# Performance work log

Hardware: AMD Instinct MI355X
Metric: run time of the kernel (lower is better)

## Reference

```python
import jax, jax.numpy as jnp
import numpy as np

B, S, HID, NH = 2, 2048, 1024, 16
HD = HID // NH  # head dim = 64


def setup_inputs() -> dict:
    key = jax.random.key(0)
    ks = jax.random.split(key, 8)
    sc = 0.02
    return {
        "hidden_states": jax.random.normal(ks[0], (B, S, HID), jnp.float32),
        "hidden_states2": jax.random.normal(ks[1], (B, S, HID), jnp.float32),
        "Wq": jax.random.normal(ks[2], (HID, HID), jnp.float32) * sc,
        "bq": jnp.zeros((HID,), jnp.float32),
        "Wk": jax.random.normal(ks[3], (HID, HID), jnp.float32) * sc,
        "bk": jnp.zeros((HID,), jnp.float32),
        "Wv": jax.random.normal(ks[4], (HID, HID), jnp.float32) * sc,
        "bv": jnp.zeros((HID,), jnp.float32),
    }


def _split_heads(x):
    # [B, S, HID] -> [B, NH, S, HD]
    b, s, _ = x.shape
    return x.reshape(b, s, NH, HD).transpose(0, 2, 1, 3)


def reference(hidden_states, hidden_states2, Wq, bq, Wk, bk, Wv, bv):
    # Linear layers use torch convention: y = x @ W.T + b
    q = _split_heads(hidden_states @ Wq.T + bq)    # [B,NH,Sq,HD]
    k = _split_heads(hidden_states2 @ Wk.T + bk)   # [B,NH,Sk,HD]
    v = _split_heads(hidden_states2 @ Wv.T + bv)   # [B,NH,Sk,HD]
    scores = jnp.einsum("bhqd,bhkd->bhqk", q, k) / jnp.sqrt(jnp.float32(HD))
    probs = jax.nn.softmax(scores, axis=-1)        # dropout prob = 0 (eval)
    ctx = jnp.einsum("bhqk,bhkd->bhqd", probs, v)  # [B,NH,Sq,HD]
    ctx = ctx.transpose(0, 2, 1, 3).reshape(hidden_states.shape[0], hidden_states.shape[1], HID)
    return ctx
```

## Files before the change

### kernel.cpp

```cpp
#include <hip/hip_runtime.h>
#include <hip/hip_bf16.h>
#include <stdint.h>

#define B_   2
#define S_   2048
#define HID_ 1024
#define NH_  16
#define HD_  64

typedef __attribute__((ext_vector_type(4))) float f32x4;
typedef __attribute__((ext_vector_type(8))) short bf16x8;

__device__ inline unsigned short f2bf(float x) {
    __hip_bfloat16 h = __float2bfloat16(x);
    return reinterpret_cast<unsigned short&>(h);
}

__device__ inline void gload_lds16(const void* g, void* l) {
    __builtin_amdgcn_global_load_lds(
        (const __attribute__((address_space(1))) void*)g,
        (__attribute__((address_space(3))) void*)l, 16, 0, 0);
}

__device__ inline float fast_exp2(float x) {
    float r;
    asm("v_exp_f32 %0, %1" : "=v"(r) : "v"(x));
    return r;
}

__global__ __launch_bounds__(256) void cvt_all(
    const float* __restrict__ X1, const float* __restrict__ X2,
    const float* __restrict__ Wq, const float* __restrict__ Wk, const float* __restrict__ Wv,
    unsigned short* __restrict__ X1b, unsigned short* __restrict__ X2b,
    unsigned short* __restrict__ Wqb, unsigned short* __restrict__ Wkb,
    unsigned short* __restrict__ Wvb)
{
    const int id = blockIdx.x;
    const float* src;
    unsigned short* dst;
    int base;
    if (id < 2048)      { src = X1; dst = X1b; base = id; }
    else if (id < 4096) { src = X2; dst = X2b; base = id - 2048; }
    else if (id < 4608) { src = Wq; dst = Wqb; base = id - 4096; }
    else if (id < 5120) { src = Wk; dst = Wkb; base = id - 4608; }
    else                { src = Wv; dst = Wvb; base = id - 5120; }
    const size_t off = (size_t)base * 2048 + (size_t)threadIdx.x * 8;
    float4 a = *(const float4*)&src[off];
    float4 b = *(const float4*)&src[off + 4];
    unsigned short o[8] = {f2bf(a.x), f2bf(a.y), f2bf(a.z), f2bf(a.w),
                           f2bf(b.x), f2bf(b.y), f2bf(b.z), f2bf(b.w)};
    *(uint4*)&dst[off] = *(uint4*)o;
}

__global__ __launch_bounds__(256, 3) void qkv_gemm(
    const unsigned short* __restrict__ X1b, const unsigned short* __restrict__ X2b,
    const unsigned short* __restrict__ Wqb, const unsigned short* __restrict__ Wkb,
    const unsigned short* __restrict__ Wvb,
    const float* __restrict__ bq, const float* __restrict__ bk, const float* __restrict__ bv,
    unsigned short* __restrict__ Qo, unsigned short* __restrict__ Ko, unsigned short* __restrict__ Vo)
{
    const int z = blockIdx.z;
    const unsigned short* X = (z == 0) ? X1b : X2b;
    const unsigned short* W = (z == 0) ? Wqb : (z == 1 ? Wkb : Wvb);
    const float* bias = (z == 0) ? bq : (z == 1 ? bk : bv);
    unsigned short* out = (z == 0) ? Qo : (z == 1 ? Ko : Vo);

    __shared__ __align__(16) unsigned short SM[128 * 132];
    unsigned short* As = SM;
    unsigned short* Bs = SM + 128 * 64;

    const int m0 = blockIdx.x * 128;
    const int n0 = blockIdx.y * 128;
    const int t = threadIdx.x;
    const int lane = t & 63;
    const int w = t >> 6;
    const int lo = lane & 15, hi = lane >> 4;
    const int wm = w >> 1, wn = w & 1;

    const int srow = lane >> 3;
    const int scol = ((lane & 7) ^ srow) * 8;

    f32x4 acc[4][4];
    const f32x4 fzero = {0.f, 0.f, 0.f, 0.f};
    #pragma unroll
    for (int i = 0; i < 4; ++i)
        #pragma unroll
        for (int j = 0; j < 4; ++j) acc[i][j] = fzero;

    for (int kt = 0; kt < 16; ++kt) {
        __syncthreads();
        #pragma unroll
        for (int i = 0; i < 4; ++i) {
            const int r = w * 32 + i * 8 + srow;
            gload_lds16(&X[(size_t)(m0 + r) * HID_ + kt * 64 + scol],
                        &As[w * 2048 + i * 512]);
            gload_lds16(&W[(size_t)(n0 + r) * HID_ + kt * 64 + scol],
                        &Bs[w * 2048 + i * 512]);
        }
        __syncthreads();

        #pragma unroll
        for (int s = 0; s < 2; ++s) {
            const int rcol = ((s * 4 + hi) ^ (lo & 7)) * 8;
            bf16x8 a[4], b[4];
            #pragma unroll
            for (int i = 0; i < 4; ++i) {
                a[i] = *(const bf16x8*)&As[(wm * 64 + i * 16 + lo) * 64 + rcol];
                b[i] = *(const bf16x8*)&Bs[(wn * 64 + i * 16 + lo) * 64 + rcol];
            }
            #pragma unroll
            for (int i = 0; i < 4; ++i)
                #pragma unroll
                for (int j = 0; j < 4; ++j)
                    acc[i][j] = __builtin_amdgcn_mfma_f32_16x16x32_bf16(a[i], b[j], acc[i][j], 0, 0, 0);
        }
    }

    if (z != 2) {
        const float sc = (z == 0) ? 0.18033688011112042f : 1.0f;
        #pragma unroll
        for (int i = 0; i < 4; ++i) {
            #pragma unroll
            for (int j = 0; j < 4; ++j) {
                int col = n0 + wn * 64 + j * 16 + lo;
                float bb = bias[col];
                #pragma unroll
                for (int r = 0; r < 4; ++r) {
                    int row = m0 + wm * 64 + i * 16 + hi * 4 + r;
                    out[(size_t)row * HID_ + col] = f2bf((acc[i][j][r] + bb) * sc);
                }
            }
        }
    } else {
        __syncthreads();
        unsigned short* Ts = SM;
        #pragma unroll
        for (int i = 0; i < 4; ++i) {
            #pragma unroll
            for (int j = 0; j < 4; ++j) {
                int nl = wn * 64 + j * 16 + lo;
                float bb = bias[n0 + nl];
                int ml = wm * 64 + i * 16 + hi * 4;
                ushort4 pk;
                pk.x = f2bf(acc[i][j][0] + bb);
                pk.y = f2bf(acc[i][j][1] + bb);
                pk.z = f2bf(acc[i][j][2] + bb);
                pk.w = f2bf(acc[i][j][3] + bb);
                *(ushort4*)&Ts[nl * 132 + ml] = pk;
            }
        }
        __syncthreads();
        const int nn = t >> 1;
        const int mh = (t & 1) * 64;
        const int bI = m0 >> 11;
        const int sb = (m0 & 2047) + mh;
        size_t obase = (size_t)bI * ((size_t)HID_ * S_) + (size_t)(n0 + nn) * S_ + sb;
        #pragma unroll
        for (int kk = 0; kk < 8; ++kk)
            *(uint4*)&out[obase + kk * 8] = *(const uint4*)&Ts[nn * 132 + mh + kk * 8];
    }
}

__global__ __launch_bounds__(256, 2) void attn_fwd(
    const unsigned short* __restrict__ Q, const unsigned short* __restrict__ K,
    const unsigned short* __restrict__ Vt, float* __restrict__ out)
{
    __shared__ __align__(16) unsigned short Ks[2][64 * 64];
    __shared__ __align__(16) unsigned short Vs[2][64 * 64];

    const int t = threadIdx.x;
    const int lane = t & 63;
    const int w = t >> 6;
    const int lo = lane & 15, hi = lane >> 4;

    const int id = blockIdx.x + 16 * blockIdx.y;
    const int vb = (id & 7) * 64 + (id >> 3);
    const int qt = vb & 15;
    const int bh = vb >> 4;
    const int b = bh >> 4, h = bh & 15;

    const int q0 = qt * 128;
    const size_t baseQK = (size_t)b * S_ * HID_ + (size_t)h * HD_;
    const size_t baseV  = (size_t)b * ((size_t)HID_ * S_) + (size_t)h * ((size_t)HD_ * S_);

    bf16x8 qb[2][2];
    #pragma unroll
    for (int qf = 0; qf < 2; ++qf)
        #pragma unroll
        for (int st = 0; st < 2; ++st)
            qb[qf][st] = *(const bf16x8*)&Q[baseQK + (size_t)(q0 + w * 32 + qf * 16 + lo) * HID_
                                            + st * 32 + hi * 8];

    f32x4 O[2][4];
    const f32x4 fzero = {0.f, 0.f, 0.f, 0.f};
    f32x4 lacc[2] = {fzero, fzero};
    #pragma unroll
    for (int qf = 0; qf < 2; ++qf)
        #pragma unroll
        for (int c = 0; c < 4; ++c) O[qf][c] = fzero;

    bf16x8 ones;
    #pragma unroll
    for (int j = 0; j < 4; ++j) ((unsigned*)&ones)[j] = 0x3F803F80u;

    const int srow = lane >> 3;
    const int scol = ((lane & 7) ^ srow) * 8;

    auto STAGE = [&](int buf, int kn) {
        #pragma unroll
        for (int i = 0; i < 2; ++i) {
            const int rr = w * 16 + i * 8 + srow;
            gload_lds16(&K[baseQK + (size_t)(kn + rr) * HID_ + scol],
                        &Ks[buf][w * 1024 + i * 512]);
            gload_lds16(&Vt[baseV + (size_t)rr * S_ + kn + scol],
                        &Vs[buf][w * 1024 + i * 512]);
        }
    };

    STAGE(0, 0);

    for (int tt = 0; tt < 32; ++tt) {
        const int cur = tt & 1;
        const bool pre = (tt < 31);

        __builtin_amdgcn_s_barrier();
        if (pre) STAGE(cur ^ 1, (tt + 1) * 64);

        if (pre) asm volatile("s_waitcnt vmcnt(4)" ::: "memory");
        else     asm volatile("s_waitcnt vmcnt(0)" ::: "memory");
        __builtin_amdgcn_s_barrier();
        __builtin_amdgcn_sched_barrier(0);

        const unsigned short* Kc = Ks[cur];
        const unsigned short* Vc = Vs[cur];

        f32x4 s[2][4];
        __builtin_amdgcn_s_setprio(1);
        #pragma unroll
        for (int n = 0; n < 4; ++n) {
            const int rc0 = (hi ^ (lo & 7)) * 8;
            const int rc1 = ((4 + hi) ^ (lo & 7)) * 8;
            bf16x8 ka0 = *(const bf16x8*)&Kc[(n * 16 + lo) * 64 + rc0];
            bf16x8 ka1 = *(const bf16x8*)&Kc[(n * 16 + lo) * 64 + rc1];
            #pragma unroll
            for (int qf = 0; qf < 2; ++qf) {
                f32x4 z = fzero;
                z = __builtin_amdgcn_mfma_f32_16x16x32_bf16(ka0, qb[qf][0], z, 0, 0, 0);
                s[qf][n] = __builtin_amdgcn_mfma_f32_16x16x32_bf16(ka1, qb[qf][1], z, 0, 0, 0);
            }
        }
        __builtin_amdgcn_s_setprio(0);

        bf16x8 pa[2][2];
        #pragma unroll
        for (int qf = 0; qf < 2; ++qf) {
            #pragma unroll
            for (int n = 0; n < 4; ++n)
                #pragma unroll
                for (int r = 0; r < 4; ++r) s[qf][n][r] = fast_exp2(s[qf][n][r]);

            unsigned pw0[4], pw1[4];
            #pragma unroll
            for (int p = 0; p < 2; ++p) {
                unsigned X, Y;
                asm("v_cvt_pk_bf16_f32 %0, %1, %2"
                    : "=v"(X) : "v"(s[qf][0][2 * p]), "v"(s[qf][0][2 * p + 1]));
                asm("v_cvt_pk_bf16_f32 %0, %1, %2"
                    : "=v"(Y) : "v"(s[qf][1][2 * p]), "v"(s[qf][1][2 * p + 1]));
                asm volatile("v_permlane32_swap_b32 %0, %1" : "+v"(X), "+v"(Y));
                asm volatile("v_permlane16_swap_b32 %0, %1" : "+v"(X), "+v"(Y));
                pw0[p] = X;
                pw0[p + 2] = Y;
            }
            #pragma unroll
            for (int p = 0; p < 2; ++p) {
                unsigned X, Y;
                asm("v_cvt_pk_bf16_f32 %0, %1, %2"
                    : "=v"(X) : "v"(s[qf][2][2 * p]), "v"(s[qf][2][2 * p + 1]));
                asm("v_cvt_pk_bf16_f32 %0, %1, %2"
                    : "=v"(Y) : "v"(s[qf][3][2 * p]), "v"(s[qf][3][2 * p + 1]));
                asm volatile("v_permlane32_swap_b32 %0, %1" : "+v"(X), "+v"(Y));
                asm volatile("v_permlane16_swap_b32 %0, %1" : "+v"(X), "+v"(Y));
                pw1[p] = X;
                pw1[p + 2] = Y;
            }
            #pragma unroll
            for (int j = 0; j < 4; ++j) {
                ((unsigned*)&pa[qf][0])[j] = pw0[j];
                ((unsigned*)&pa[qf][1])[j] = pw1[j];
            }
        }

        __builtin_amdgcn_s_setprio(1);
        #pragma unroll
        for (int c = 0; c < 4; ++c) {
            const int rc0 = (hi ^ (lo & 7)) * 8;
            const int rc1 = ((4 + hi) ^ (lo & 7)) * 8;
            bf16x8 vb0 = *(const bf16x8*)&Vc[(c * 16 + lo) * 64 + rc0];
            bf16x8 vb1 = *(const bf16x8*)&Vc[(c * 16 + lo) * 64 + rc1];
            #pragma unroll
            for (int qf = 0; qf < 2; ++qf) {
                O[qf][c] = __builtin_amdgcn_mfma_f32_16x16x32_bf16(pa[qf][0], vb0, O[qf][c], 0, 0, 0);
                O[qf][c] = __builtin_amdgcn_mfma_f32_16x16x32_bf16(pa[qf][1], vb1, O[qf][c], 0, 0, 0);
            }
        }
        #pragma unroll
        for (int qf = 0; qf < 2; ++qf) {
            lacc[qf] = __builtin_amdgcn_mfma_f32_16x16x32_bf16(pa[qf][0], ones, lacc[qf], 0, 0, 0);
            lacc[qf] = __builtin_amdgcn_mfma_f32_16x16x32_bf16(pa[qf][1], ones, lacc[qf], 0, 0, 0);
        }
        __builtin_amdgcn_s_setprio(0);
    }

    #pragma unroll
    for (int qf = 0; qf < 2; ++qf) {
        float linv[4];
        #pragma unroll
        for (int r = 0; r < 4; ++r) linv[r] = 1.0f / lacc[qf][r];
        #pragma unroll
        for (int c = 0; c < 4; ++c) {
            #pragma unroll
            for (int r = 0; r < 4; ++r) {
                int q = q0 + w * 32 + qf * 16 + hi * 4 + r;
                out[(size_t)b * S_ * HID_ + (size_t)q * HID_ + h * HD_ + c * 16 + lo] =
                    O[qf][c][r] * linv[r];
            }
        }
    }
}

extern "C" void kernel_launch(void* const* d_in, const int* in_sizes, int n_in,
                              void* d_out, int out_size, void* d_ws, size_t ws_size,
                              hipStream_t stream) {
    const float* hs1 = (const float*)d_in[0];
    const float* hs2 = (const float*)d_in[1];
    const float* Wq  = (const float*)d_in[2];
    const float* bq  = (const float*)d_in[3];
    const float* Wk  = (const float*)d_in[4];
    const float* bk  = (const float*)d_in[5];
    const float* Wv  = (const float*)d_in[6];
    const float* bv  = (const float*)d_in[7];
    float* out = (float*)d_out;

    const size_t XY = (size_t)B_ * S_ * HID_;
    const size_t WW = (size_t)HID_ * HID_;
    unsigned short* Qb  = (unsigned short*)d_ws;
    unsigned short* Kb  = Qb + XY;
    unsigned short* Vb  = Kb + XY;
    unsigned short* X1b = Vb + XY;
    unsigned short* X2b = X1b + XY;
    unsigned short* Wqb = X2b + XY;
    unsigned short* Wkb = Wqb + WW;
    unsigned short* Wvb = Wkb + WW;

    cvt_all<<<5632, 256, 0, stream>>>(hs1, hs2, Wq, Wk, Wv, X1b, X2b, Wqb, Wkb, Wvb);
    qkv_gemm<<<dim3(32, 8, 3), 256, 0, stream>>>(X1b, X2b, Wqb, Wkb, Wvb,
                                                 bq, bk, bv, Qb, Kb, Vb);
    attn_fwd<<<dim3(16, 32), 256, 0, stream>>>(Qb, Kb, Vb, out);
}
```

Baseline: 86.88 us.

## Enlarge QKV GEMM tile to 256x256 with 512 threads and double-buffered LDS

The QKV projection GEMM moves from 128x128 tiles with 256 threads to 256x256 tiles with 8 waves. K-tile loads are double-buffered in 128KB of LDS, so the next global-to-LDS copy overlaps the current MFMA work. Larger tiles give more reuse per loaded byte but shrink the grid from 768 to 192 blocks, which can leave many CUs idle on a 256-CU part. The V-transpose epilogue is split into two passes so it fits the staging buffer.

```diff
diff --git a/kernel.cpp b/kernel.cpp
--- a/kernel.cpp
+++ b/kernel.cpp
@@ -52,7 +52,7 @@
     *(uint4*)&dst[off] = *(uint4*)o;
 }
 
-__global__ __launch_bounds__(256, 3) void qkv_gemm(
+__global__ __launch_bounds__(512, 1) void qkv_gemm(
     const unsigned short* __restrict__ X1b, const unsigned short* __restrict__ X2b,
     const unsigned short* __restrict__ Wqb, const unsigned short* __restrict__ Wkb,
     const unsigned short* __restrict__ Wvb,
@@ -65,99 +65,128 @@
     const float* bias = (z == 0) ? bq : (z == 1 ? bk : bv);
     unsigned short* out = (z == 0) ? Qo : (z == 1 ? Ko : Vo);
 
-    __shared__ __align__(16) unsigned short SM[128 * 132];
-    unsigned short* As = SM;
-    unsigned short* Bs = SM + 128 * 64;
-
-    const int m0 = blockIdx.x * 128;
-    const int n0 = blockIdx.y * 128;
+    __shared__ __align__(16) unsigned short SM[65536];
+
     const int t = threadIdx.x;
     const int lane = t & 63;
     const int w = t >> 6;
     const int lo = lane & 15, hi = lane >> 4;
-    const int wm = w >> 1, wn = w & 1;
-
-    const int srow = lane >> 3;
-    const int scol = ((lane & 7) ^ srow) * 8;
-
-    f32x4 acc[4][4];
+    const int wm = w >> 2, wn = w & 3;
+
+    const int m0 = blockIdx.x * 256;
+    const int n0 = blockIdx.y * 256;
+
+    const int srow8 = lane >> 3;
+    const int sslot = (lane & 7) ^ srow8;
+
+    f32x4 acc[8][4];
     const f32x4 fzero = {0.f, 0.f, 0.f, 0.f};
     #pragma unroll
-    for (int i = 0; i < 4; ++i)
+    for (int i = 0; i < 8; ++i)
         #pragma unroll
         for (int j = 0; j < 4; ++j) acc[i][j] = fzero;
 
+    auto STAGE = [&](int buf, int kt) {
+        unsigned short* Ab = SM + buf * 32768;
+        unsigned short* Bb = Ab + 16384;
+        #pragma unroll
+        for (int s2 = 0; s2 < 4; ++s2) {
+            const int r = s2 * 64 + w * 8 + srow8;
+            gload_lds16(&X[(size_t)(m0 + r) * HID_ + kt * 64 + sslot * 8],
+                        &Ab[(s2 * 64 + w * 8) * 64]);
+            gload_lds16(&W[(size_t)(n0 + r) * HID_ + kt * 64 + sslot * 8],
+                        &Bb[(s2 * 64 + w * 8) * 64]);
+        }
+    };
+
+    STAGE(0, 0);
+
     for (int kt = 0; kt < 16; ++kt) {
-        __syncthreads();
-        #pragma unroll
-        for (int i = 0; i < 4; ++i) {
-            const int r = w * 32 + i * 8 + srow;
-            gload_lds16(&X[(size_t)(m0 + r) * HID_ + kt * 64 + scol],
-                        &As[w * 2048 + i * 512]);
-            gload_lds16(&W[(size_t)(n0 + r) * HID_ + kt * 64 + scol],
-                        &Bs[w * 2048 + i * 512]);
-        }
-        __syncthreads();
-
-        #pragma unroll
-        for (int s = 0; s < 2; ++s) {
-            const int rcol = ((s * 4 + hi) ^ (lo & 7)) * 8;
-            bf16x8 a[4], b[4];
-            #pragma unroll
-            for (int i = 0; i < 4; ++i) {
-                a[i] = *(const bf16x8*)&As[(wm * 64 + i * 16 + lo) * 64 + rcol];
-                b[i] = *(const bf16x8*)&Bs[(wn * 64 + i * 16 + lo) * 64 + rcol];
-            }
-            #pragma unroll
-            for (int i = 0; i < 4; ++i)
-                #pragma unroll
-                for (int j = 0; j < 4; ++j)
-                    acc[i][j] = __builtin_amdgcn_mfma_f32_16x16x32_bf16(a[i], b[j], acc[i][j], 0, 0, 0);
-        }
+        const int cur = kt & 1;
+
+        asm volatile("s_waitcnt vmcnt(0)" ::: "memory");
+        __builtin_amdgcn_s_barrier();
+        __builtin_amdgcn_sched_barrier(0);
+
+        if (kt < 15) STAGE(cur ^ 1, kt + 1);
+
+        const unsigned short* Ab = SM + cur * 32768;
+        const unsigned short* Bb = Ab + 16384;
+
+        bf16x8 bfr[4][2];
+        #pragma unroll
+        for (int j = 0; j < 4; ++j) {
+            const int rb = wn * 64 + j * 16 + lo;
+            #pragma unroll
+            for (int kk = 0; kk < 2; ++kk) {
+                const int slot = (kk * 4 + hi) ^ (lo & 7);
+                bfr[j][kk] = *(const bf16x8*)&Bb[rb * 64 + slot * 8];
+            }
+        }
+        __builtin_amdgcn_s_setprio(1);
+        #pragma unroll
+        for (int i = 0; i < 8; ++i) {
+            const int ra = wm * 128 + i * 16 + lo;
+            const int s0 = hi ^ (lo & 7);
+            const int s1 = (4 + hi) ^ (lo & 7);
+            bf16x8 a0 = *(const bf16x8*)&Ab[ra * 64 + s0 * 8];
+            bf16x8 a1 = *(const bf16x8*)&Ab[ra * 64 + s1 * 8];
+            #pragma unroll
+            for (int j = 0; j < 4; ++j) {
+                acc[i][j] = __builtin_amdgcn_mfma_f32_16x16x32_bf16(a0, bfr[j][0], acc[i][j], 0, 0, 0);
+                acc[i][j] = __builtin_amdgcn_mfma_f32_16x16x32_bf16(a1, bfr[j][1], acc[i][j], 0, 0, 0);
+            }
+        }
+        __builtin_amdgcn_s_setprio(0);
     }
 
     if (z != 2) {
         const float sc = (z == 0) ? 0.18033688011112042f : 1.0f;
         #pragma unroll
-        for (int i = 0; i < 4; ++i) {
+        for (int i = 0; i < 8; ++i) {
             #pragma unroll
             for (int j = 0; j < 4; ++j) {
                 int col = n0 + wn * 64 + j * 16 + lo;
                 float bb = bias[col];
                 #pragma unroll
                 for (int r = 0; r < 4; ++r) {
-                    int row = m0 + wm * 64 + i * 16 + hi * 4 + r;
+                    int row = m0 + wm * 128 + i * 16 + hi * 4 + r;
                     out[(size_t)row * HID_ + col] = f2bf((acc[i][j][r] + bb) * sc);
                 }
             }
         }
     } else {
-        __syncthreads();
         unsigned short* Ts = SM;
-        #pragma unroll
-        for (int i = 0; i < 4; ++i) {
-            #pragma unroll
-            for (int j = 0; j < 4; ++j) {
-                int nl = wn * 64 + j * 16 + lo;
-                float bb = bias[n0 + nl];
-                int ml = wm * 64 + i * 16 + hi * 4;
-                ushort4 pk;
-                pk.x = f2bf(acc[i][j][0] + bb);
-                pk.y = f2bf(acc[i][j][1] + bb);
-                pk.z = f2bf(acc[i][j][2] + bb);
-                pk.w = f2bf(acc[i][j][3] + bb);
-                *(ushort4*)&Ts[nl * 132 + ml] = pk;
-            }
-        }
-        __syncthreads();
-        const int nn = t >> 1;
-        const int mh = (t & 1) * 64;
         const int bI = m0 >> 11;
-        const int sb = (m0 & 2047) + mh;
-        size_t obase = (size_t)bI * ((size_t)HID_ * S_) + (size_t)(n0 + nn) * S_ + sb;
-        #pragma unroll
-        for (int kk = 0; kk < 8; ++kk)
-            *(uint4*)&out[obase + kk * 8] = *(const uint4*)&Ts[nn * 132 + mh + kk * 8];
+        #pragma unroll
+        for (int pass = 0; pass < 2; ++pass) {
+            __builtin_amdgcn_s_barrier();
+            if (wm == pass) {
+                #pragma unroll
+                for (int i = 0; i < 8; ++i) {
+                    #pragma unroll
+                    for (int j = 0; j < 4; ++j) {
+                        int nl = wn * 64 + j * 16 + lo;
+                        float bb = bias[n0 + nl];
+                        int ml = i * 16 + hi * 4;
+                        ushort4 pk;
+                        pk.x = f2bf(acc[i][j][0] + bb);
+                        pk.y = f2bf(acc[i][j][1] + bb);
+                        pk.z = f2bf(acc[i][j][2] + bb);
+                        pk.w = f2bf(acc[i][j][3] + bb);
+                        *(ushort4*)&Ts[nl * 132 + ml] = pk;
+                    }
+                }
+            }
+            __builtin_amdgcn_s_barrier();
+            const int nn = t >> 1;
+            const int mh = (t & 1) * 64;
+            const int sb = (m0 & 2047) + pass * 128 + mh;
+            size_t obase = (size_t)bI * ((size_t)HID_ * S_) + (size_t)(n0 + nn) * S_ + sb;
+            #pragma unroll
+            for (int kk = 0; kk < 8; ++kk)
+                *(uint4*)&out[obase + kk * 8] = *(const uint4*)&Ts[nn * 132 + mh + kk * 8];
+        }
     }
 }
 
@@ -244,9 +273,9 @@
             bf16x8 ka1 = *(const bf16x8*)&Kc[(n * 16 + lo) * 64 + rc1];
             #pragma unroll
             for (int qf = 0; qf < 2; ++qf) {
-                f32x4 z = fzero;
-                z = __builtin_amdgcn_mfma_f32_16x16x32_bf16(ka0, qb[qf][0], z, 0, 0, 0);
-                s[qf][n] = __builtin_amdgcn_mfma_f32_16x16x32_bf16(ka1, qb[qf][1], z, 0, 0, 0);
+                f32x4 zc = fzero;
+                zc = __builtin_amdgcn_mfma_f32_16x16x32_bf16(ka0, qb[qf][0], zc, 0, 0, 0);
+                s[qf][n] = __builtin_amdgcn_mfma_f32_16x16x32_bf16(ka1, qb[qf][1], zc, 0, 0, 0);
             }
         }
         __builtin_amdgcn_s_setprio(0);
@@ -354,7 +383,7 @@
     unsigned short* Wvb = Wkb + WW;
 
     cvt_all<<<5632, 256, 0, stream>>>(hs1, hs2, Wq, Wk, Wv, X1b, X2b, Wqb, Wkb, Wvb);
-    qkv_gemm<<<dim3(32, 8, 3), 256, 0, stream>>>(X1b, X2b, Wqb, Wkb, Wvb,
+    qkv_gemm<<<dim3(16, 4, 3), 512, 0, stream>>>(X1b, X2b, Wqb, Wkb, Wvb,
                                                  bq, bk, bv, Qb, Kb, Vb);
     attn_fwd<<<dim3(16, 32), 256, 0, stream>>>(Qb, Kb, Vb, out);
 }
```

Result: slower. 94.36 us (+8.6%).
